# Kernel optimization log

Hardware: AMD Instinct MI355X
Metric: run time of the kernel (lower is better)

## Reference

```python
import jax, jax.numpy as jnp
import numpy as np

B, S, D = 2, 2048, 1024
H = 16
HD = D // H  # 64


def _xavier(key, shape):
    fan_out, fan_in = shape
    limit = np.sqrt(6.0 / (fan_in + fan_out)).astype(np.float32)
    return jax.random.uniform(key, shape, jnp.float32, -limit, limit)


def setup_inputs() -> dict:
    key = jax.random.key(0)
    ks = jax.random.split(key, 6)
    return {
        "x": jax.random.normal(ks[0], (B, S, D), jnp.float32),
        "pos_bias": jax.random.normal(ks[1], (1, H, S, S), jnp.float32) * 0.02,
        "sinusoidal_pos": jax.random.normal(ks[2], (1, 1, S, HD), jnp.float32),
        "mask": jax.random.randint(ks[3], (1, 1, S, S), 0, 2, jnp.int32),
        "W_qkv": _xavier(ks[4], (3 * D, D)),
        "b_qkv": jnp.zeros((3 * D,), jnp.float32),
        "W_o": _xavier(ks[5], (D, D)),
        "b_o": jnp.zeros((D,), jnp.float32),
    }


def _rotate_half(t):
    # t: [..., HD]; reshape to [..., 2, HD//2], swap halves with sign flip
    t2 = t.reshape(*t.shape[:-1], 2, HD // 2)
    a, b = t2[..., 0, :], t2[..., 1, :]
    return jnp.concatenate((-b, a), axis=-1)


def _apply_rope(t, sinusoidal_pos):
    sp = sinusoidal_pos[:, :, -t.shape[-2]:]
    return t * jnp.cos(sp) + _rotate_half(t) * jnp.sin(sp)


def reference(x, pos_bias, sinusoidal_pos, mask, W_qkv, b_qkv, W_o, b_o):
    b, s, _ = x.shape
    qkv = x @ W_qkv.T + b_qkv                     # [B,S,3D]
    qkv = qkv.reshape(b, s, H, 3 * HD).transpose(0, 2, 1, 3)  # [B,H,S,3hd]
    q, k, v = jnp.split(qkv, 3, axis=-1)
    q = _apply_rope(q, sinusoidal_pos)
    k = _apply_rope(k, sinusoidal_pos)
    logits = jnp.einsum("bhqd,bhkd->bhqk", q, k)  # [B,H,S,S]
    logits = (logits + pos_bias) / np.sqrt(HD).astype(np.float32)
    logits = jnp.where(mask == 0, jnp.float32(-9e15), logits)
    attn = jax.nn.softmax(logits, axis=-1)
    vals = jnp.einsum("bhqk,bhkd->bhqd", attn, v)
    vals = vals.transpose(0, 2, 1, 3).reshape(b, s, D)
    return vals @ W_o.T + b_o
```

## Files before the change

kernel.cpp:

```cpp
#include <hip/hip_runtime.h>
#include <cmath>

#define B_ 2
#define S_ 2048
#define D_ 1024
#define H_ 16
#define HD_ 64

typedef __attribute__((ext_vector_type(8))) short bf16x8;
typedef __attribute__((ext_vector_type(4))) short bf16x4;
typedef __attribute__((ext_vector_type(4))) float floatx4;
#define MFMA_BF16(a, b, c) __builtin_amdgcn_mfma_f32_16x16x32_bf16(a, b, c, 0, 0, 0)

__device__ __forceinline__ ushort f2bf(float x) {
    union { float f; unsigned u; } v; v.f = x;
    unsigned u = v.u;
    return (ushort)((u + 0x7FFFu + ((u >> 16) & 1u)) >> 16);
}
__device__ __forceinline__ float bf2f(ushort b) {
    union { unsigned u; float f; } v; v.u = ((unsigned)b) << 16;
    return v.f;
}

__global__ __launch_bounds__(256) void f32_split_bf16(
    const float* __restrict__ in, ushort* __restrict__ hi,
    ushort* __restrict__ lo, int n4)
{
    int i = blockIdx.x * 256 + threadIdx.x;
    if (i >= n4) return;
    float4 v = ((const float4*)in)[i];
    bf16x4 h, l;
    float vv[4] = {v.x, v.y, v.z, v.w};
#pragma unroll
    for (int j = 0; j < 4; ++j) {
        ushort hb = f2bf(vv[j]);
        h[j] = (short)hb;
        l[j] = (short)f2bf(vv[j] - bf2f(hb));
    }
    ((bf16x4*)hi)[i] = h;
    ((bf16x4*)lo)[i] = l;
}

__global__ __launch_bounds__(256, 2) void gemm_mfma_split(
    const ushort* __restrict__ Ah, const ushort* __restrict__ Al,
    const ushort* __restrict__ Wh, const ushort* __restrict__ Wl,
    const float* __restrict__ bias, float* __restrict__ C,
    int M, int N, int K)
{
    constexpr int LD = 40;
    __shared__ ushort Ash[128][LD], Asl[128][LD], Wsh[128][LD], Wsl[128][LD];

    const int tid = threadIdx.x;
    const int lane = tid & 63;
    const int wv = tid >> 6;
    const int l15 = lane & 15;
    const int quad = lane >> 4;
    const int bm = blockIdx.y * 128;
    const int bn = blockIdx.x * 128;
    const int mw = (wv & 1) * 64;
    const int nw = (wv >> 1) * 64;

    floatx4 acc[4][4];
#pragma unroll
    for (int i = 0; i < 4; ++i)
#pragma unroll
        for (int j = 0; j < 4; ++j) acc[i][j] = (floatx4){0.f, 0.f, 0.f, 0.f};

    const int srow = tid >> 2;
    const int sc8 = (tid & 3) * 8;

    bf16x8 pAh[2], pAl[2], pWh[2], pWl[2];
    auto fetch = [&](int k0) {
#pragma unroll
        for (int u = 0; u < 2; ++u) {
            int r = srow + u * 64;
            pAh[u] = *(const bf16x8*)(Ah + (size_t)(bm + r) * K + k0 + sc8);
            pAl[u] = *(const bf16x8*)(Al + (size_t)(bm + r) * K + k0 + sc8);
            pWh[u] = *(const bf16x8*)(Wh + (size_t)(bn + r) * K + k0 + sc8);
            pWl[u] = *(const bf16x8*)(Wl + (size_t)(bn + r) * K + k0 + sc8);
        }
    };

    fetch(0);
    for (int k0 = 0; k0 < K; k0 += 32) {
        __syncthreads();
#pragma unroll
        for (int u = 0; u < 2; ++u) {
            int r = srow + u * 64;
            *(bf16x8*)&Ash[r][sc8] = pAh[u];
            *(bf16x8*)&Asl[r][sc8] = pAl[u];
            *(bf16x8*)&Wsh[r][sc8] = pWh[u];
            *(bf16x8*)&Wsl[r][sc8] = pWl[u];
        }
        __syncthreads();
        if (k0 + 32 < K) fetch(k0 + 32);

        bf16x8 aH[4], aL[4], bH[4], bL[4];
#pragma unroll
        for (int f = 0; f < 4; ++f) {
            aH[f] = *(const bf16x8*)&Ash[mw + f * 16 + l15][quad * 8];
            aL[f] = *(const bf16x8*)&Asl[mw + f * 16 + l15][quad * 8];
            bH[f] = *(const bf16x8*)&Wsh[nw + f * 16 + l15][quad * 8];
            bL[f] = *(const bf16x8*)&Wsl[nw + f * 16 + l15][quad * 8];
        }
#pragma unroll
        for (int mf = 0; mf < 4; ++mf)
#pragma unroll
            for (int nf = 0; nf < 4; ++nf) {
                acc[mf][nf] = MFMA_BF16(aH[mf], bH[nf], acc[mf][nf]);
                acc[mf][nf] = MFMA_BF16(aH[mf], bL[nf], acc[mf][nf]);
                acc[mf][nf] = MFMA_BF16(aL[mf], bH[nf], acc[mf][nf]);
            }
    }

#pragma unroll
    for (int mf = 0; mf < 4; ++mf)
#pragma unroll
        for (int nf = 0; nf < 4; ++nf) {
            int col = bn + nw + nf * 16 + l15;
            float bv = bias[col];
#pragma unroll
            for (int reg = 0; reg < 4; ++reg) {
                int row = bm + mw + mf * 16 + quad * 4 + reg;
                C[(size_t)row * N + col] = acc[mf][nf][reg] + bv;
            }
        }
}

__global__ __launch_bounds__(256) void rope_split_bf16(
    const float* __restrict__ qkv, const float* __restrict__ sp,
    ushort* __restrict__ q_hi, ushort* __restrict__ q_lo,
    ushort* __restrict__ k_hi, ushort* __restrict__ k_lo,
    ushort* __restrict__ v_t)
{
    __shared__ ushort VT[64][72];
    const int s0 = blockIdx.x * 64;
    const int h = blockIdx.y;
    const int b = blockIdx.z;
    const int d = threadIdx.x & 63;
    const int sw = threadIdx.x >> 6;
    const float sgn = (d < 32) ? -1.f : 1.f;

#pragma unroll 4
    for (int i = 0; i < 16; ++i) {
        int sl = i * 4 + sw;
        int s = s0 + sl;
        size_t base = ((size_t)(b * S_ + s)) * (3 * D_) + h * (3 * HD_) + d;
        float tq = qkv[base];
        float tk = qkv[base + HD_];
        float tv = qkv[base + 2 * HD_];
        float spv = sp[s * HD_ + d];
        float c = cosf(spv), sn = sinf(spv);
        float pq = __shfl_xor(tq, 32);
        float pk = __shfl_xor(tk, 32);
        float qv = (tq * c + sgn * pq * sn) * 0.125f;
        float kv = tk * c + sgn * pk * sn;

        size_t o = ((size_t)((b * H_ + h) * S_ + s)) * HD_ + d;
        ushort qh = f2bf(qv);
        q_hi[o] = qh; q_lo[o] = f2bf(qv - bf2f(qh));
        ushort kh = f2bf(kv);
        k_hi[o] = kh; k_lo[o] = f2bf(kv - bf2f(kh));
        VT[d][sl] = f2bf(tv);
    }
    __syncthreads();
    const int dd = threadIdx.x >> 2;
    const int c0 = (threadIdx.x & 3) * 16;
    size_t ob = ((size_t)((b * H_ + h) * HD_ + dd)) * S_ + s0 + c0;
    *(bf16x8*)(v_t + ob)     = *(const bf16x8*)&VT[dd][c0];
    *(bf16x8*)(v_t + ob + 8) = *(const bf16x8*)&VT[dd][c0 + 8];
}

__global__ __launch_bounds__(256, 3) void attn_flash_v3(
    const ushort* __restrict__ q_hi, const ushort* __restrict__ q_lo,
    const ushort* __restrict__ k_hi, const ushort* __restrict__ k_lo,
    const ushort* __restrict__ v_t, const float* __restrict__ pb,
    const int* __restrict__ mask,
    ushort* __restrict__ vals_hi, ushort* __restrict__ vals_lo)
{
    __shared__ ushort Kh[64][72];
    __shared__ ushort Kl[64][72];
    __shared__ ushort Vt[64][72];
    __shared__ ushort PBM[64][76];
    __shared__ ushort Ps[4][16][72];

    const int tid = threadIdx.x;
    const int lane = tid & 63;
    const int wv = tid >> 6;
    const int l15 = lane & 15;
    const int quad = lane >> 4;
    const int q0 = blockIdx.x * 64;
    const int h = blockIdx.y;
    const int b = blockIdx.z;
    const int qbase = q0 + wv * 16;

    const size_t bh_sd = ((size_t)(b * H_ + h)) * (size_t)S_ * HD_;

    const ushort* qrow_h = q_hi + bh_sd + (size_t)(qbase + l15) * HD_;
    const ushort* qrow_l = q_lo + bh_sd + (size_t)(qbase + l15) * HD_;
    bf16x8 qA_h0 = *(const bf16x8*)(qrow_h + quad * 8);
    bf16x8 qA_h1 = *(const bf16x8*)(qrow_h + 32 + quad * 8);
    bf16x8 qA_l0 = *(const bf16x8*)(qrow_l + quad * 8);
    bf16x8 qA_l1 = *(const bf16x8*)(qrow_l + 32 + quad * 8);

    floatx4 O4[4];
    float l_[4];
#pragma unroll
    for (int f = 0; f < 4; ++f) O4[f] = (floatx4){0.f, 0.f, 0.f, 0.f};
#pragma unroll
    for (int r = 0; r < 4; ++r) l_[r] = 0.f;

    const int kr = tid >> 3;
    const int kc8 = (tid & 7) * 8;
    const int pr = tid >> 4;
    const int pc4 = (tid & 15) * 4;

    bf16x8 pKh[2], pKl[2], pVt[2];
    float4 pPb[4];
    int4 pMk[4];
    auto fetch = [&](int kt) {
#pragma unroll
        for (int u = 0; u < 2; ++u) {
            int r = kr + u * 32;
            pKh[u] = *(const bf16x8*)(k_hi + bh_sd + (size_t)(kt + r) * HD_ + kc8);
            pKl[u] = *(const bf16x8*)(k_lo + bh_sd + (size_t)(kt + r) * HD_ + kc8);
            pVt[u] = *(const bf16x8*)(v_t + bh_sd + (size_t)r * S_ + kt + kc8);
        }
#pragma unroll
        for (int u = 0; u < 4; ++u) {
            int r = pr + u * 16;
            pPb[u] = *(const float4*)(pb + ((size_t)h * S_ + q0 + r) * S_ + kt + pc4);
            pMk[u] = *(const int4*)(mask + (size_t)(q0 + r) * S_ + kt + pc4);
        }
    };

    fetch(0);
    for (int kt = 0; kt < S_; kt += 64) {
        __syncthreads();
#pragma unroll
        for (int u = 0; u < 2; ++u) {
            int r = kr + u * 32;
            *(bf16x8*)&Kh[r][kc8] = pKh[u];
            *(bf16x8*)&Kl[r][kc8] = pKl[u];
            *(bf16x8*)&Vt[r][kc8] = pVt[u];
        }
#pragma unroll
        for (int u = 0; u < 4; ++u) {
            int r = pr + u * 16;
            bf16x4 w;
            w[0] = (short)f2bf(pMk[u].x == 0 ? -9e15f : pPb[u].x * 0.125f);
            w[1] = (short)f2bf(pMk[u].y == 0 ? -9e15f : pPb[u].y * 0.125f);
            w[2] = (short)f2bf(pMk[u].z == 0 ? -9e15f : pPb[u].z * 0.125f);
            w[3] = (short)f2bf(pMk[u].w == 0 ? -9e15f : pPb[u].w * 0.125f);
            *(bf16x4*)&PBM[r][pc4] = w;
        }
        __syncthreads();
        if (kt + 64 < S_) fetch(kt + 64);

        floatx4 S4[4];
#pragma unroll
        for (int nf = 0; nf < 4; ++nf) {
            const int krow = nf * 16 + l15;
            bf16x8 bh0 = *(const bf16x8*)&Kh[krow][quad * 8];
            bf16x8 bh1 = *(const bf16x8*)&Kh[krow][32 + quad * 8];
            bf16x8 bl0 = *(const bf16x8*)&Kl[krow][quad * 8];
            bf16x8 bl1 = *(const bf16x8*)&Kl[krow][32 + quad * 8];
            floatx4 a = (floatx4){0.f, 0.f, 0.f, 0.f};
            a = MFMA_BF16(qA_h0, bh0, a);
            a = MFMA_BF16(qA_h1, bh1, a);
            a = MFMA_BF16(qA_h0, bl0, a);
            a = MFMA_BF16(qA_h1, bl1, a);
            a = MFMA_BF16(qA_l0, bh0, a);
            a = MFMA_BF16(qA_l1, bh1, a);
            S4[nf] = a;
        }

#pragma unroll
        for (int nf = 0; nf < 4; ++nf) {
#pragma unroll
            for (int reg = 0; reg < 4; ++reg) {
                float x = S4[nf][reg] +
                    bf2f(PBM[wv * 16 + quad * 4 + reg][nf * 16 + l15]);
                float p = __expf(x);
                l_[reg] += p;
                Ps[wv][quad * 4 + reg][nf * 16 + l15] = f2bf(p);
            }
        }

        bf16x8 pA0 = *(const bf16x8*)&Ps[wv][l15][quad * 8];
        bf16x8 pA1 = *(const bf16x8*)&Ps[wv][l15][32 + quad * 8];
#pragma unroll
        for (int df = 0; df < 4; ++df) {
            const int vrow = df * 16 + l15;
            bf16x8 vB0 = *(const bf16x8*)&Vt[vrow][quad * 8];
            bf16x8 vB1 = *(const bf16x8*)&Vt[vrow][32 + quad * 8];
            O4[df] = MFMA_BF16(pA0, vB0, O4[df]);
            O4[df] = MFMA_BF16(pA1, vB1, O4[df]);
        }
    }

#pragma unroll
    for (int reg = 0; reg < 4; ++reg) {
        float lv = l_[reg];
        lv += __shfl_xor(lv, 1);
        lv += __shfl_xor(lv, 2);
        lv += __shfl_xor(lv, 4);
        lv += __shfl_xor(lv, 8);
        float inv = 1.f / lv;
        const int row = qbase + quad * 4 + reg;
        size_t ob = ((size_t)(b * S_ + row)) * D_ + h * HD_;
#pragma unroll
        for (int df = 0; df < 4; ++df) {
            float o = O4[df][reg] * inv;
            ushort hb = f2bf(o);
            vals_hi[ob + df * 16 + l15] = hb;
            vals_lo[ob + df * 16 + l15] = f2bf(o - bf2f(hb));
        }
    }
}

extern "C" void kernel_launch(void* const* d_in, const int* in_sizes, int n_in,
                              void* d_out, int out_size, void* d_ws, size_t ws_size,
                              hipStream_t stream) {
    const float* x      = (const float*)d_in[0];
    const float* pos_b  = (const float*)d_in[1];
    const float* sp     = (const float*)d_in[2];
    const int*   mask   = (const int*)d_in[3];
    const float* W_qkv  = (const float*)d_in[4];
    const float* b_qkv  = (const float*)d_in[5];
    const float* W_o    = (const float*)d_in[6];
    const float* b_o    = (const float*)d_in[7];
    float* out = (float*)d_out;

    char* w = (char*)d_ws;
    float*  qkv   = (float*)w;   w += (size_t)4096 * 3072 * 4;
    ushort* xv_hi = (ushort*)w;  w += (size_t)4096 * 1024 * 2;
    ushort* xv_lo = (ushort*)w;  w += (size_t)4096 * 1024 * 2;
    ushort* wq_hi = (ushort*)w;  w += (size_t)3072 * 1024 * 2;
    ushort* wq_lo = (ushort*)w;  w += (size_t)3072 * 1024 * 2;
    ushort* wo_hi = (ushort*)w;  w += (size_t)1024 * 1024 * 2;
    ushort* wo_lo = (ushort*)w;  w += (size_t)1024 * 1024 * 2;
    ushort* q_hi  = (ushort*)w;  w += (size_t)B_ * H_ * S_ * HD_ * 2;
    ushort* q_lo  = (ushort*)w;  w += (size_t)B_ * H_ * S_ * HD_ * 2;
    ushort* k_hi  = (ushort*)w;  w += (size_t)B_ * H_ * S_ * HD_ * 2;
    ushort* k_lo  = (ushort*)w;  w += (size_t)B_ * H_ * S_ * HD_ * 2;
    ushort* v_t   = (ushort*)w;  w += (size_t)B_ * H_ * S_ * HD_ * 2;

    f32_split_bf16<<<4096, 256, 0, stream>>>(x, xv_hi, xv_lo, 4096 * 1024 / 4);
    f32_split_bf16<<<3072, 256, 0, stream>>>(W_qkv, wq_hi, wq_lo, 3072 * 1024 / 4);
    f32_split_bf16<<<1024, 256, 0, stream>>>(W_o, wo_hi, wo_lo, 1024 * 1024 / 4);

    gemm_mfma_split<<<dim3(3072 / 128, 4096 / 128), 256, 0, stream>>>(
        xv_hi, xv_lo, wq_hi, wq_lo, b_qkv, qkv, 4096, 3072, 1024);

    rope_split_bf16<<<dim3(S_ / 64, H_, B_), 256, 0, stream>>>(
        qkv, sp, q_hi, q_lo, k_hi, k_lo, v_t);

    attn_flash_v3<<<dim3(S_ / 64, H_, B_), 256, 0, stream>>>(
        q_hi, q_lo, k_hi, k_lo, v_t, pos_b, mask, xv_hi, xv_lo);

    gemm_mfma_split<<<dim3(1024 / 128, 4096 / 128), 256, 0, stream>>>(
        xv_hi, xv_lo, wo_hi, wo_lo, b_o, out, 4096, 1024, 1024);
}
```

Before: 645.4 us.

## Load GEMM tiles directly to LDS and remap attention grid batch order

The GEMM now uses global_load_lds to copy 16-byte fragments straight into LDS in an MFMA-fragment-major layout, which removes the register-staged prefetch and the padded row layout. Each lane then reads its fragment contiguously. The kernel raises the occupancy hint to 3 blocks per CU, but it loses the overlap of the next tile's fetch with compute and needs an extra barrier per k-step. The attention grid folds the batch into blockIdx.x so that the two batches of the same head are scheduled close together, which may improve L2 reuse of pos_bias.

```diff
diff --git a/kernel.cpp b/kernel.cpp
--- a/kernel.cpp
+++ b/kernel.cpp
@@ -20,6 +20,12 @@
 __device__ __forceinline__ float bf2f(ushort b) {
     union { unsigned u; float f; } v; v.u = ((unsigned)b) << 16;
     return v.f;
+}
+
+__device__ __forceinline__ void g2l16(const ushort* g, ushort* l) {
+    __builtin_amdgcn_global_load_lds(
+        (const __attribute__((address_space(1))) unsigned int*)g,
+        (__attribute__((address_space(3))) unsigned int*)l, 16, 0, 0);
 }
 
 __global__ __launch_bounds__(256) void f32_split_bf16(
@@ -41,14 +47,13 @@
     ((bf16x4*)lo)[i] = l;
 }
 
-__global__ __launch_bounds__(256, 2) void gemm_mfma_split(
+__global__ __launch_bounds__(256, 3) void gemm_mfma_v2(
     const ushort* __restrict__ Ah, const ushort* __restrict__ Al,
     const ushort* __restrict__ Wh, const ushort* __restrict__ Wl,
     const float* __restrict__ bias, float* __restrict__ C,
     int M, int N, int K)
 {
-    constexpr int LD = 40;
-    __shared__ ushort Ash[128][LD], Asl[128][LD], Wsh[128][LD], Wsl[128][LD];
+    __shared__ ushort AhB[8 * 512], AlB[8 * 512], WhB[8 * 512], WlB[8 * 512];
 
     const int tid = threadIdx.x;
     const int lane = tid & 63;
@@ -59,6 +64,18 @@
     const int bn = blockIdx.x * 128;
     const int mw = (wv & 1) * 64;
     const int nw = (wv >> 1) * 64;
+    const int mf0 = mw >> 4;
+    const int nf0 = nw >> 4;
+
+    const int f0 = wv * 2;
+    const ushort* gA0 = Ah + (size_t)(bm + f0 * 16 + l15) * K + quad * 8;
+    const ushort* gA1 = Ah + (size_t)(bm + f0 * 16 + 16 + l15) * K + quad * 8;
+    const ushort* gAl0 = Al + (size_t)(bm + f0 * 16 + l15) * K + quad * 8;
+    const ushort* gAl1 = Al + (size_t)(bm + f0 * 16 + 16 + l15) * K + quad * 8;
+    const ushort* gW0 = Wh + (size_t)(bn + f0 * 16 + l15) * K + quad * 8;
+    const ushort* gW1 = Wh + (size_t)(bn + f0 * 16 + 16 + l15) * K + quad * 8;
+    const ushort* gWl0 = Wl + (size_t)(bn + f0 * 16 + l15) * K + quad * 8;
+    const ushort* gWl1 = Wl + (size_t)(bn + f0 * 16 + 16 + l15) * K + quad * 8;
 
     floatx4 acc[4][4];
 #pragma unroll
@@ -66,42 +83,24 @@
 #pragma unroll
         for (int j = 0; j < 4; ++j) acc[i][j] = (floatx4){0.f, 0.f, 0.f, 0.f};
 
-    const int srow = tid >> 2;
-    const int sc8 = (tid & 3) * 8;
-
-    bf16x8 pAh[2], pAl[2], pWh[2], pWl[2];
-    auto fetch = [&](int k0) {
-#pragma unroll
-        for (int u = 0; u < 2; ++u) {
-            int r = srow + u * 64;
-            pAh[u] = *(const bf16x8*)(Ah + (size_t)(bm + r) * K + k0 + sc8);
-            pAl[u] = *(const bf16x8*)(Al + (size_t)(bm + r) * K + k0 + sc8);
-            pWh[u] = *(const bf16x8*)(Wh + (size_t)(bn + r) * K + k0 + sc8);
-            pWl[u] = *(const bf16x8*)(Wl + (size_t)(bn + r) * K + k0 + sc8);
-        }
-    };
-
-    fetch(0);
     for (int k0 = 0; k0 < K; k0 += 32) {
+        g2l16(gA0 + k0, AhB + (f0 + 0) * 512);
+        g2l16(gA1 + k0, AhB + (f0 + 1) * 512);
+        g2l16(gAl0 + k0, AlB + (f0 + 0) * 512);
+        g2l16(gAl1 + k0, AlB + (f0 + 1) * 512);
+        g2l16(gW0 + k0, WhB + (f0 + 0) * 512);
+        g2l16(gW1 + k0, WhB + (f0 + 1) * 512);
+        g2l16(gWl0 + k0, WlB + (f0 + 0) * 512);
+        g2l16(gWl1 + k0, WlB + (f0 + 1) * 512);
         __syncthreads();
-#pragma unroll
-        for (int u = 0; u < 2; ++u) {
-            int r = srow + u * 64;
-            *(bf16x8*)&Ash[r][sc8] = pAh[u];
-            *(bf16x8*)&Asl[r][sc8] = pAl[u];
-            *(bf16x8*)&Wsh[r][sc8] = pWh[u];
-            *(bf16x8*)&Wsl[r][sc8] = pWl[u];
-        }
-        __syncthreads();
-        if (k0 + 32 < K) fetch(k0 + 32);
 
         bf16x8 aH[4], aL[4], bH[4], bL[4];
 #pragma unroll
         for (int f = 0; f < 4; ++f) {
-            aH[f] = *(const bf16x8*)&Ash[mw + f * 16 + l15][quad * 8];
-            aL[f] = *(const bf16x8*)&Asl[mw + f * 16 + l15][quad * 8];
-            bH[f] = *(const bf16x8*)&Wsh[nw + f * 16 + l15][quad * 8];
-            bL[f] = *(const bf16x8*)&Wsl[nw + f * 16 + l15][quad * 8];
+            aH[f] = *(const bf16x8*)(AhB + (mf0 + f) * 512 + lane * 8);
+            aL[f] = *(const bf16x8*)(AlB + (mf0 + f) * 512 + lane * 8);
+            bH[f] = *(const bf16x8*)(WhB + (nf0 + f) * 512 + lane * 8);
+            bL[f] = *(const bf16x8*)(WlB + (nf0 + f) * 512 + lane * 8);
         }
 #pragma unroll
         for (int mf = 0; mf < 4; ++mf)
@@ -111,6 +110,7 @@
                 acc[mf][nf] = MFMA_BF16(aH[mf], bL[nf], acc[mf][nf]);
                 acc[mf][nf] = MFMA_BF16(aL[mf], bH[nf], acc[mf][nf]);
             }
+        __syncthreads();
     }
 
 #pragma unroll
@@ -171,7 +171,7 @@
     *(bf16x8*)(v_t + ob + 8) = *(const bf16x8*)&VT[dd][c0 + 8];
 }
 
-__global__ __launch_bounds__(256, 3) void attn_flash_v3(
+__global__ __launch_bounds__(256, 3) void attn_flash_v4(
     const ushort* __restrict__ q_hi, const ushort* __restrict__ q_lo,
     const ushort* __restrict__ k_hi, const ushort* __restrict__ k_lo,
     const ushort* __restrict__ v_t, const float* __restrict__ pb,
@@ -189,9 +189,9 @@
     const int wv = tid >> 6;
     const int l15 = lane & 15;
     const int quad = lane >> 4;
-    const int q0 = blockIdx.x * 64;
+    const int b = blockIdx.x >> 5;
+    const int q0 = (blockIdx.x & 31) * 64;
     const int h = blockIdx.y;
-    const int b = blockIdx.z;
     const int qbase = q0 + wv * 16;
 
     const size_t bh_sd = ((size_t)(b * H_ + h)) * (size_t)S_ * HD_;
@@ -350,15 +350,15 @@
     f32_split_bf16<<<3072, 256, 0, stream>>>(W_qkv, wq_hi, wq_lo, 3072 * 1024 / 4);
     f32_split_bf16<<<1024, 256, 0, stream>>>(W_o, wo_hi, wo_lo, 1024 * 1024 / 4);
 
-    gemm_mfma_split<<<dim3(3072 / 128, 4096 / 128), 256, 0, stream>>>(
+    gemm_mfma_v2<<<dim3(3072 / 128, 4096 / 128), 256, 0, stream>>>(
         xv_hi, xv_lo, wq_hi, wq_lo, b_qkv, qkv, 4096, 3072, 1024);
 
     rope_split_bf16<<<dim3(S_ / 64, H_, B_), 256, 0, stream>>>(
         qkv, sp, q_hi, q_lo, k_hi, k_lo, v_t);
 
-    attn_flash_v3<<<dim3(S_ / 64, H_, B_), 256, 0, stream>>>(
+    attn_flash_v4<<<dim3(2 * (S_ / 64), H_), 256, 0, stream>>>(
         q_hi, q_lo, k_hi, k_lo, v_t, pos_b, mask, xv_hi, xv_lo);
 
-    gemm_mfma_split<<<dim3(1024 / 128, 4096 / 128), 256, 0, stream>>>(
+    gemm_mfma_v2<<<dim3(1024 / 128, 4096 / 128), 256, 0, stream>>>(
         xv_hi, xv_lo, wo_hi, wo_lo, b_o, out, 4096, 1024, 1024);
 }
```

Result: slower. 677.4 us (+5.0%).
